# Kernel optimization log

Hardware: AMD Instinct MI355X
Metric: run time of the kernel (lower is better)

## Reference

```python
import jax, jax.numpy as jnp
import numpy as np

TEMP = 1.0
PRIOR = 0.2
THRESHOLD = 0.5
EPS = 1.1920929e-07  # torch float32 eps used by probs_to_logits / clamp_probs


def setup_inputs() -> dict:
    key = jax.random.key(0)
    k1, k2, k3, k4, k5 = jax.random.split(key, 5)
    B, L, D = 8, 8192, 256
    hidden = jax.random.normal(k1, (B, L, D), dtype=jnp.float32)
    # q/k projections are initialized to identity in the module; perturb slightly
    Wq = jnp.eye(D, dtype=jnp.float32) + 0.02 * jax.random.normal(k2, (D, D), dtype=jnp.float32)
    Wk = jnp.eye(D, dtype=jnp.float32) + 0.02 * jax.random.normal(k3, (D, D), dtype=jnp.float32)
    # uniform noise for the RelaxedBernoulli reparameterized sample
    noise = jax.random.uniform(k4, (B, L), dtype=jnp.float32)
    # ragged lengths -> contiguous attention mask (1s then 0s), as the module assumes
    lengths = jax.random.randint(k5, (B,), L // 2, L + 1)
    attention_mask = (jnp.arange(L)[None, :] < lengths[:, None]).astype(jnp.float32)
    return {"hidden": hidden, "Wq": Wq, "Wk": Wk, "noise": noise, "attention_mask": attention_mask}


def _binomial_loss(k, n, p):
    # -log Binomial(n, p).log_prob(k) / n
    logp = (jax.scipy.special.gammaln(n + 1.0)
            - jax.scipy.special.gammaln(k + 1.0)
            - jax.scipy.special.gammaln(n - k + 1.0)
            + k * jnp.log(p) + (n - k) * jnp.log1p(-p))
    return -logp / n


def reference(hidden, Wq, Wk, noise, attention_mask):
    B, L, D = hidden.shape
    # F.normalize along last dim (eps=1e-12), then linear projections (no bias)
    hn = hidden / jnp.maximum(jnp.linalg.norm(hidden, axis=-1, keepdims=True), 1e-12)
    q = jnp.einsum('bld,ed->ble', hn[:, :-1], Wq)
    k = jnp.einsum('bld,ed->ble', hn[:, 1:], Wk)
    cos_sim = jnp.sum(q * k, axis=-1)                      # [B, L-1]
    probs = jnp.clip((1.0 - cos_sim) * 0.5, 0.0, 1.0)
    probs = jnp.pad(probs, ((0, 0), (1, 0)), constant_values=1.0)  # boundary forced at t=0

    # RelaxedBernoulli(temp, probs).rsample() with externally supplied uniforms
    p = jnp.clip(probs, EPS, 1.0 - EPS)
    logits = jnp.log(p) - jnp.log1p(-p)
    u = jnp.clip(noise, EPS, 1.0 - EPS)
    soft = jax.nn.sigmoid((logits + jnp.log(u) - jnp.log1p(-u)) / TEMP)
    hard = (soft > THRESHOLD).astype(soft.dtype)
    hard = jax.lax.stop_gradient(hard - soft) + soft       # straight-through

    # mask out boundaries in padding; force a boundary at the last real token
    hard = hard * attention_mask
    pad_mask = attention_mask == 0
    first_pad = pad_mask & (jnp.cumsum(pad_mask.astype(jnp.int32), axis=1) == 1)
    last_real = jnp.roll(first_pad, shift=-1, axis=1).at[:, -1].set(False)
    hard = jnp.maximum(hard, last_real.astype(hard.dtype))

    # downsample: mean-pool tokens within each boundary-delimited segment.
    # boundary==1 starts a new segment; segment id = cumsum(hard) - 1.
    hard_bin = jax.lax.stop_gradient(hard) > 0.5
    seg = jnp.cumsum(hard_bin.astype(jnp.int32), axis=1) - 1
    seg = jnp.clip(seg, 0, L - 1)
    flat_seg = (seg + jnp.arange(B, dtype=jnp.int32)[:, None] * L).reshape(-1)  # [B*L]
    w = attention_mask.reshape(-1)                                              # pads excluded
    sums = jax.ops.segment_sum(hidden.reshape(-1, D) * w[:, None], flat_seg, num_segments=B * L)
    cnts = jax.ops.segment_sum(w, flat_seg, num_segments=B * L)
    pooled = (sums / (cnts + 1e-9)[:, None]).reshape(B, L, D)  # [B, S_max<=L, D], zero-padded

    n_b = jnp.sum(hard, axis=1)                  # boundaries per batch row
    num_boundaries = jnp.sum(n_b)
    total_positions = jnp.sum(attention_mask)
    # gathered mask values at kept positions are all 1 -> prefix-ones of length n_b
    shortened_attention_mask = (jnp.arange(L)[None, :]
                                < jax.lax.stop_gradient(n_b)[:, None]).astype(jnp.float32)
    loss = _binomial_loss(num_boundaries, total_positions, PRIOR)
    return pooled, loss, num_boundaries, total_positions, shortened_attention_mask
```

## Files before the change

### kernel.cpp

```cpp
#include <hip/hip_runtime.h>
#include <hip/hip_bf16.h>
#include <math.h>

#define L_SEQ 8192
#define B_BATCH 8
#define D_DIM 256
#define BL (B_BATCH * L_SEQ)
#define EPS_F 1.1920929e-07f

typedef __attribute__((ext_vector_type(8))) short short8;
typedef __attribute__((ext_vector_type(4))) float f32x4;
typedef __attribute__((ext_vector_type(4))) unsigned short u16x4;


__device__ inline unsigned short f2bf(float x) {
    __hip_bfloat16 b = __float2bfloat16(x);
    return *(unsigned short*)&b;
}
__device__ inline float bf2f(unsigned short u) {
    __hip_bfloat16 b = *(__hip_bfloat16*)&u;
    return __bfloat162float(b);
}

__global__ __launch_bounds__(256) void k_matMpack(
    const float* __restrict__ Wq, const float* __restrict__ Wk,
    unsigned short* __restrict__ Bpack) {
    __shared__ float Aq[64][33];
    __shared__ float Ak[64][17];
    const int f   = blockIdx.x;
    const int k8  = f >> 4, ct = f & 15;
    const int tid = threadIdx.x;
    const int n   = tid & 15;
    const int k   = tid >> 4;
    float a0 = 0.f, a1 = 0.f;
    for (int e0 = 0; e0 < 256; e0 += 64) {
        for (int i = tid; i < 64 * 32; i += 256) {
            const int e = i >> 5, d = i & 31;
            Aq[e][d] = Wq[(e0 + e) * 256 + k8 * 32 + d];
        }
        for (int i = tid; i < 64 * 16; i += 256) {
            const int e = i >> 4, d = i & 15;
            Ak[e][d] = Wk[(e0 + e) * 256 + ct * 16 + d];
        }
        __syncthreads();
#pragma unroll 8
        for (int e = 0; e < 64; ++e) {
            a0 += Aq[e][k] * Ak[e][n];
            a1 += Aq[e][k + 16] * Ak[e][n];
        }
        __syncthreads();
    }
    const int col = ct * 16 + n;
    const float M0 = a0 - ((k8 * 32 + k)      == col ? 1.0f : 0.0f);
    const float M1 = a1 - ((k8 * 32 + k + 16) == col ? 1.0f : 0.0f);
    const unsigned short h0 = f2bf(M0), h1 = f2bf(M1);
    const unsigned short l0 = f2bf(M0 - bf2f(h0)), l1 = f2bf(M1 - bf2f(h1));
    unsigned short* dstH = Bpack + (size_t)(k8 * 16 + ct) * 512;
    unsigned short* dstL = dstH + 128 * 512;
    const int q0 = k >> 3, j0 = k & 7;
    const int q1 = (k + 16) >> 3;
    dstH[(q0 * 16 + n) * 8 + j0] = h0;
    dstH[(q1 * 16 + n) * 8 + j0] = h1;
    dstL[(q0 * 16 + n) * 8 + j0] = l0;
    dstL[(q1 * 16 + n) * 8 + j0] = l1;
}

#define RS 264
#define MM(A,Bv,C) __builtin_amdgcn_mfma_f32_16x16x32_bf16((A),(Bv),(C),0,0,0)
#define MFMA16(V0,V1,V2,V3,BN) \
    acc[0][0]=MM(V0,BN##_0,acc[0][0]); acc[0][1]=MM(V0,BN##_1,acc[0][1]); \
    acc[0][2]=MM(V0,BN##_2,acc[0][2]); acc[0][3]=MM(V0,BN##_3,acc[0][3]); \
    acc[1][0]=MM(V1,BN##_0,acc[1][0]); acc[1][1]=MM(V1,BN##_1,acc[1][1]); \
    acc[1][2]=MM(V1,BN##_2,acc[1][2]); acc[1][3]=MM(V1,BN##_3,acc[1][3]); \
    acc[2][0]=MM(V2,BN##_0,acc[2][0]); acc[2][1]=MM(V2,BN##_1,acc[2][1]); \
    acc[2][2]=MM(V2,BN##_2,acc[2][2]); acc[2][3]=MM(V2,BN##_3,acc[2][3]); \
    acc[3][0]=MM(V3,BN##_0,acc[3][0]); acc[3][1]=MM(V3,BN##_1,acc[3][1]); \
    acc[3][2]=MM(V3,BN##_2,acc[3][2]); acc[3][3]=MM(V3,BN##_3,acc[3][3]);
#define LOADB(BN,S) \
    BN##_0 = Bld[(((S) * 16) + w4 + 0) * 64]; \
    BN##_1 = Bld[(((S) * 16) + w4 + 1) * 64]; \
    BN##_2 = Bld[(((S) * 16) + w4 + 2) * 64]; \
    BN##_3 = Bld[(((S) * 16) + w4 + 3) * 64];
#define STRIP_HL(S,BN) { \
    const int co = ((S) & 7) * 32; \
    const short8 hv0 = *(const short8*)(hA0 + co), hv1 = *(const short8*)(hA1 + co), \
                 hv2 = *(const short8*)(hA2 + co), hv3 = *(const short8*)(hA3 + co); \
    const short8 lv0 = *(const short8*)(lA0 + co), lv1 = *(const short8*)(lA1 + co), \
                 lv2 = *(const short8*)(lA2 + co), lv3 = *(const short8*)(lA3 + co); \
    MFMA16(hv0,hv1,hv2,hv3,BN); \
    MFMA16(lv0,lv1,lv2,lv3,BN); \
    LOADB(BN,(S)+3); }
#define STRIP_H(S,BN) { \
    const int co = ((S) & 7) * 32; \
    const short8 hv0 = *(const short8*)(hA0 + co), hv1 = *(const short8*)(hA1 + co), \
                 hv2 = *(const short8*)(hA2 + co), hv3 = *(const short8*)(hA3 + co); \
    MFMA16(hv0,hv1,hv2,hv3,BN); \
    if ((S) + 3 < 16) { LOADB(BN,(S)+3); } }

__global__ __launch_bounds__(256, 2) void k_cosmfma(
    const float* __restrict__ hidden, const unsigned short* __restrict__ Bpack,
    const float* __restrict__ noise, unsigned char* __restrict__ hard) {
    __shared__ __attribute__((aligned(16))) unsigned short hiA[65 * RS];
    __shared__ __attribute__((aligned(16))) unsigned short loA[65 * RS];
    __shared__ float Vpart[4][64];
    __shared__ float dots[64];

    const int tid  = threadIdx.x;
    const int lane = tid & 63;
    const int w    = tid >> 6;
    const int w16  = w * 16;
    const int w4   = w * 4;
    const int T0   = blockIdx.x * 64;

    const short8* __restrict__ Bld = (const short8*)Bpack + lane;

    short8 bA_0, bA_1, bA_2, bA_3, bB_0, bB_1, bB_2, bB_3, bC_0, bC_1, bC_2, bC_3;
    LOADB(bA, 0);
    LOADB(bB, 1);
    LOADB(bC, 2);

    {
        int tokA = T0 - 1 + w16; if (tokA < 0) tokA = 0;
        float4 vb0 = ((const float4*)hidden)[(size_t)tokA * 64 + lane];
        float4 vb1 = ((const float4*)hidden)[(size_t)(T0 + w16) * 64 + lane];
        float4 hp4 = {0.f, 0.f, 0.f, 0.f};
#pragma unroll 1
        for (int ii = 0; ii <= 16; ++ii) {
            const float4 vcur = vb0;
            vb0 = vb1;
            if (ii + 2 <= 16)
                vb1 = ((const float4*)hidden)[(size_t)(T0 + w16 + ii + 1) * 64 + lane];
            float ss = vcur.x * vcur.x + vcur.y * vcur.y + vcur.z * vcur.z + vcur.w * vcur.w;
#pragma unroll
            for (int sh = 32; sh >= 1; sh >>= 1) ss += __shfl_xor(ss, sh);
            const float inv = 1.0f / fmaxf(sqrtf(ss), 1e-12f);
            float4 h4;
            h4.x = vcur.x * inv; h4.y = vcur.y * inv;
            h4.z = vcur.z * inv; h4.w = vcur.w * inv;
            const unsigned short hx = f2bf(h4.x), hy = f2bf(h4.y),
                                 hz = f2bf(h4.z), hw2 = f2bf(h4.w);
            const u16x4 hv4 = {hx, hy, hz, hw2};
            const u16x4 lv4 = {f2bf(h4.x - bf2f(hx)), f2bf(h4.y - bf2f(hy)),
                               f2bf(h4.z - bf2f(hz)), f2bf(h4.w - bf2f(hw2))};
            const int i = w16 + ii;
            *(u16x4*)&hiA[i * RS + lane * 4] = hv4;
            *(u16x4*)&loA[i * RS + lane * 4] = lv4;
            if (ii > 0) {
                float pd = h4.x * hp4.x + h4.y * hp4.y + h4.z * hp4.z + h4.w * hp4.w;
#pragma unroll
                for (int sh = 32; sh >= 1; sh >>= 1) pd += __shfl_xor(pd, sh);
                if (lane == 0) dots[i - 1] = pd;
            }
            hp4 = h4;
        }
    }
    __syncthreads();

    const int m = lane & 15, q = lane >> 4;
    const unsigned short* __restrict__ hA0 = &hiA[(0  + m) * RS + q * 8];
    const unsigned short* __restrict__ hA1 = &hiA[(16 + m) * RS + q * 8];
    const unsigned short* __restrict__ hA2 = &hiA[(32 + m) * RS + q * 8];
    const unsigned short* __restrict__ hA3 = &hiA[(48 + m) * RS + q * 8];
    const unsigned short* __restrict__ lA0 = &loA[(0  + m) * RS + q * 8];
    const unsigned short* __restrict__ lA1 = &loA[(16 + m) * RS + q * 8];
    const unsigned short* __restrict__ lA2 = &loA[(32 + m) * RS + q * 8];
    const unsigned short* __restrict__ lA3 = &loA[(48 + m) * RS + q * 8];

    f32x4 acc[4][4];
#pragma unroll
    for (int af = 0; af < 4; ++af)
#pragma unroll
        for (int c = 0; c < 4; ++c) { f32x4 z = {0.f, 0.f, 0.f, 0.f}; acc[af][c] = z; }

    STRIP_HL(0, bA)  STRIP_HL(1, bB)  STRIP_HL(2, bC)  STRIP_HL(3, bA)
    STRIP_HL(4, bB)  STRIP_HL(5, bC)  STRIP_HL(6, bA)  STRIP_HL(7, bB)
    STRIP_H (8, bC)  STRIP_H (9, bA)  STRIP_H (10, bB) STRIP_H (11, bC)
    STRIP_H (12, bA) STRIP_H (13, bB) STRIP_H (14, bC) STRIP_H (15, bA)

#pragma unroll
    for (int af = 0; af < 4; ++af) {
#pragma unroll
        for (int r = 0; r < 4; ++r) {
            const int row = af * 16 + (q << 2) + r;
            const int ib  = (row + 1) * RS + w4 * 16 + m;
            float pp = acc[af][0][r] * (bf2f(hiA[ib     ]) + bf2f(loA[ib     ]))
                     + acc[af][1][r] * (bf2f(hiA[ib + 16]) + bf2f(loA[ib + 16]))
                     + acc[af][2][r] * (bf2f(hiA[ib + 32]) + bf2f(loA[ib + 32]))
                     + acc[af][3][r] * (bf2f(hiA[ib + 48]) + bf2f(loA[ib + 48]));
            pp += __shfl_xor(pp, 1);
            pp += __shfl_xor(pp, 2);
            pp += __shfl_xor(pp, 4);
            pp += __shfl_xor(pp, 8);
            if (m == 0) Vpart[w][row] = pp;
        }
    }
    __syncthreads();
    if (lane < 16) {
        const int rl = w16 + lane;
        const float part = Vpart[0][rl] + Vpart[1][rl] + Vpart[2][rl] + Vpart[3][rl];
        const int t = T0 + rl;
        const int l = t & (L_SEQ - 1);
        float p;
        if (l == 0) {
            p = 1.0f;
        } else {
            p = (1.0f - (part + dots[rl])) * 0.5f;
            p = fminf(fmaxf(p, 0.0f), 1.0f);
        }
        p = fminf(fmaxf(p, EPS_F), 1.0f - EPS_F);
        float u = noise[t];
        u = fminf(fmaxf(u, EPS_F), 1.0f - EPS_F);
        const float z = ((logf(p) - log1pf(-p)) + logf(u)) - log1pf(-u);
        hard[t] = (z > 0.0f) ? (unsigned char)1 : (unsigned char)0;
    }
}

__global__ __launch_bounds__(1024) void k_scan(
    const float* __restrict__ mask, const unsigned char* __restrict__ hard,
    int* __restrict__ starts, int* __restrict__ nb_arr,
    int* __restrict__ len_arr, float* __restrict__ out_short) {
    __shared__ int wsum[16];
    __shared__ int s_len;
    const int b = blockIdx.x, tid = threadIdx.x;
    const int lane = tid & 63, wv = tid >> 6;
    const int base = b * L_SEQ;

    const float4* m4 = (const float4*)(mask + base);
    const float4 va = m4[tid * 2], vb = m4[tid * 2 + 1];
    int cnt = (va.x != 0.f) + (va.y != 0.f) + (va.z != 0.f) + (va.w != 0.f)
            + (vb.x != 0.f) + (vb.y != 0.f) + (vb.z != 0.f) + (vb.w != 0.f);
#pragma unroll
    for (int sh = 32; sh >= 1; sh >>= 1) cnt += __shfl_xor(cnt, sh);
    if (lane == 0) wsum[wv] = cnt;
    __syncthreads();
    if (tid == 0) {
        int s = 0;
        for (int i = 0; i < 16; ++i) s += wsum[i];
        s_len = s;
    }
    __syncthreads();
    const int len = s_len;

    const int i0 = tid * 8;
    const uint2 hb = ((const uint2*)(hard + base))[tid];
    int c = 0;
    unsigned int bits = 0;
#pragma unroll
    for (int j = 0; j < 8; ++j) {
        const unsigned int byte = ((j < 4 ? hb.x : hb.y) >> (8 * (j & 3))) & 0xffu;
        int h = ((i0 + j) < len) ? (int)(byte != 0u) : 0;
        if (len < L_SEQ && (i0 + j) == len - 1) h = 1;
        bits |= (unsigned int)h << j;
        c += h;
    }
    int x = c;
#pragma unroll
    for (int ofs = 1; ofs < 64; ofs <<= 1) {
        const int t = __shfl_up(x, ofs);
        if (lane >= ofs) x += t;
    }
    if (lane == 63) wsum[wv] = x;
    __syncthreads();
    int woff = 0, nb = 0;
#pragma unroll
    for (int i = 0; i < 16; ++i) {
        const int t = wsum[i];
        nb += t;
        if (i < wv) woff += t;
    }
    int run = woff + x - c;
#pragma unroll
    for (int j = 0; j < 8; ++j)
        if ((bits >> j) & 1u) { starts[base + run] = i0 + j; ++run; }

    if (tid == 0) { nb_arr[b] = nb; len_arr[b] = len; }

    float4 o0, o1;
    o0.x = (i0 + 0) < nb ? 1.f : 0.f; o0.y = (i0 + 1) < nb ? 1.f : 0.f;
    o0.z = (i0 + 2) < nb ? 1.f : 0.f; o0.w = (i0 + 3) < nb ? 1.f : 0.f;
    o1.x = (i0 + 4) < nb ? 1.f : 0.f; o1.y = (i0 + 5) < nb ? 1.f : 0.f;
    o1.z = (i0 + 6) < nb ? 1.f : 0.f; o1.w = (i0 + 7) < nb ? 1.f : 0.f;
    float4* os4 = (float4*)(out_short + base);
    os4[tid * 2] = o0;
    os4[tid * 2 + 1] = o1;
}

__global__ __launch_bounds__(256) void k_pool(
    const float* __restrict__ hidden, const int* __restrict__ starts,
    const int* __restrict__ nb_arr, const int* __restrict__ len_arr,
    float* __restrict__ pooled) {
    const int tid  = threadIdx.x;
    const int lane = tid & 63;
    const int wid  = blockIdx.x * 4 + (tid >> 6);
    const int b    = wid >> 13;
    const int s    = wid & (L_SEQ - 1);
    const int nb   = nb_arr[b];

    float4 res = {0.f, 0.f, 0.f, 0.f};
    if (s < nb) {
        const int start = (s == 0) ? 0 : starts[b * L_SEQ + s];
        const int end   = (s + 1 < nb) ? starts[b * L_SEQ + s + 1] : len_arr[b];
        float4 acc = {0.f, 0.f, 0.f, 0.f};
        for (int t = start; t < end; ++t) {
            const float4 v = ((const float4*)hidden)[(b * L_SEQ + t) * 64 + lane];
            acc.x += v.x; acc.y += v.y; acc.z += v.z; acc.w += v.w;
        }
        const float cntf = (float)(end - start);
        res.x = acc.x / cntf; res.y = acc.y / cntf; res.z = acc.z / cntf; res.w = acc.w / cntf;
    }
    ((float4*)pooled)[(size_t)wid * 64 + lane] = res;
}

__global__ void k_final(const int* __restrict__ nb_arr, const int* __restrict__ len_arr,
                        float* __restrict__ out_scal) {
    if (threadIdx.x == 0) {
        int nb = 0, ln = 0;
        for (int b = 0; b < B_BATCH; ++b) { nb += nb_arr[b]; ln += len_arr[b]; }
        const double k = (double)nb, n = (double)ln;
        const double logp = lgamma(n + 1.0) - lgamma(k + 1.0) - lgamma(n - k + 1.0)
                            + k * log(0.2) + (n - k) * log(0.8);
        const double loss = -logp / n;
        out_scal[0] = (float)loss;
        out_scal[1] = (float)nb;
        out_scal[2] = (float)ln;
    }
}

extern "C" void kernel_launch(void* const* d_in, const int* in_sizes, int n_in,
                              void* d_out, int out_size, void* d_ws, size_t ws_size,
                              hipStream_t stream) {
    const float* hidden = (const float*)d_in[0];
    const float* Wq     = (const float*)d_in[1];
    const float* Wk     = (const float*)d_in[2];
    const float* noise  = (const float*)d_in[3];
    const float* mask   = (const float*)d_in[4];
    float* out = (float*)d_out;
    char* ws = (char*)d_ws;

    int*            starts = (int*)(ws);
    unsigned short* Bpack  = (unsigned short*)(ws + 262144);
    unsigned char*  hard   = (unsigned char*)(ws + 524288);
    int*            nb_arr = (int*)(ws + 589824);
    int*            len_arr= (int*)(ws + 589856);

    float* pooled = out;
    float* scal   = out + (size_t)BL * D_DIM;
    float* shortm = scal + 3;

    k_matMpack<<<128, 256, 0, stream>>>(Wq, Wk, Bpack);
    k_cosmfma <<<BL / 64, 256, 0, stream>>>(hidden, Bpack, noise, hard);
    k_scan    <<<B_BATCH, 1024, 0, stream>>>(mask, hard, starts, nb_arr, len_arr, shortm);
    k_pool    <<<BL / 4, 256, 0, stream>>>(hidden, starts, nb_arr, len_arr, pooled);
    k_final   <<<1, 64, 0, stream>>>(nb_arr, len_arr, scal);
}
```

Baseline: 189.3 us.

## Split cosine MFMA block across 8 waves with 2x4 wave tiling

Raises the k_cosmfma block size from 256 to 512 threads and splits the 64-row tile between two row groups of waves, so each wave computes 32 rows by 4 column groups instead of 64 rows. The normalize/pack prologue now gives 8 tokens per wave instead of 16. The goal is more waves per CU for latency hiding and fewer accumulators per wave (acc drops from 4x4 to 2x4) so occupancy can rise. In exchange, each B fragment is loaded twice per block, by two waves, and the larger block may limit residency through LDS use.

```diff
diff --git a/kernel.cpp b/kernel.cpp
--- a/kernel.cpp
+++ b/kernel.cpp
@@ -67,37 +67,30 @@
 
 #define RS 264
 #define MM(A,Bv,C) __builtin_amdgcn_mfma_f32_16x16x32_bf16((A),(Bv),(C),0,0,0)
-#define MFMA16(V0,V1,V2,V3,BN) \
+#define MFMA8(V0,V1,BN) \
     acc[0][0]=MM(V0,BN##_0,acc[0][0]); acc[0][1]=MM(V0,BN##_1,acc[0][1]); \
     acc[0][2]=MM(V0,BN##_2,acc[0][2]); acc[0][3]=MM(V0,BN##_3,acc[0][3]); \
     acc[1][0]=MM(V1,BN##_0,acc[1][0]); acc[1][1]=MM(V1,BN##_1,acc[1][1]); \
-    acc[1][2]=MM(V1,BN##_2,acc[1][2]); acc[1][3]=MM(V1,BN##_3,acc[1][3]); \
-    acc[2][0]=MM(V2,BN##_0,acc[2][0]); acc[2][1]=MM(V2,BN##_1,acc[2][1]); \
-    acc[2][2]=MM(V2,BN##_2,acc[2][2]); acc[2][3]=MM(V2,BN##_3,acc[2][3]); \
-    acc[3][0]=MM(V3,BN##_0,acc[3][0]); acc[3][1]=MM(V3,BN##_1,acc[3][1]); \
-    acc[3][2]=MM(V3,BN##_2,acc[3][2]); acc[3][3]=MM(V3,BN##_3,acc[3][3]);
+    acc[1][2]=MM(V1,BN##_2,acc[1][2]); acc[1][3]=MM(V1,BN##_3,acc[1][3]);
 #define LOADB(BN,S) \
-    BN##_0 = Bld[(((S) * 16) + w4 + 0) * 64]; \
-    BN##_1 = Bld[(((S) * 16) + w4 + 1) * 64]; \
-    BN##_2 = Bld[(((S) * 16) + w4 + 2) * 64]; \
-    BN##_3 = Bld[(((S) * 16) + w4 + 3) * 64];
+    BN##_0 = Bld[(((S) * 16) + wc4 + 0) * 64]; \
+    BN##_1 = Bld[(((S) * 16) + wc4 + 1) * 64]; \
+    BN##_2 = Bld[(((S) * 16) + wc4 + 2) * 64]; \
+    BN##_3 = Bld[(((S) * 16) + wc4 + 3) * 64];
 #define STRIP_HL(S,BN) { \
     const int co = ((S) & 7) * 32; \
-    const short8 hv0 = *(const short8*)(hA0 + co), hv1 = *(const short8*)(hA1 + co), \
-                 hv2 = *(const short8*)(hA2 + co), hv3 = *(const short8*)(hA3 + co); \
-    const short8 lv0 = *(const short8*)(lA0 + co), lv1 = *(const short8*)(lA1 + co), \
-                 lv2 = *(const short8*)(lA2 + co), lv3 = *(const short8*)(lA3 + co); \
-    MFMA16(hv0,hv1,hv2,hv3,BN); \
-    MFMA16(lv0,lv1,lv2,lv3,BN); \
-    LOADB(BN,(S)+3); }
+    const short8 hv0 = *(const short8*)(hA0 + co), hv1 = *(const short8*)(hA1 + co); \
+    const short8 lv0 = *(const short8*)(lA0 + co), lv1 = *(const short8*)(lA1 + co); \
+    MFMA8(hv0, hv1, BN); \
+    MFMA8(lv0, lv1, BN); \
+    LOADB(BN, (S) + 3); }
 #define STRIP_H(S,BN) { \
     const int co = ((S) & 7) * 32; \
-    const short8 hv0 = *(const short8*)(hA0 + co), hv1 = *(const short8*)(hA1 + co), \
-                 hv2 = *(const short8*)(hA2 + co), hv3 = *(const short8*)(hA3 + co); \
-    MFMA16(hv0,hv1,hv2,hv3,BN); \
-    if ((S) + 3 < 16) { LOADB(BN,(S)+3); } }
-
-__global__ __launch_bounds__(256, 2) void k_cosmfma(
+    const short8 hv0 = *(const short8*)(hA0 + co), hv1 = *(const short8*)(hA1 + co); \
+    MFMA8(hv0, hv1, BN); \
+    if ((S) + 3 < 16) { LOADB(BN, (S) + 3); } }
+
+__global__ __launch_bounds__(512, 4) void k_cosmfma(
     const float* __restrict__ hidden, const unsigned short* __restrict__ Bpack,
     const float* __restrict__ noise, unsigned char* __restrict__ hard) {
     __shared__ __attribute__((aligned(16))) unsigned short hiA[65 * RS];
@@ -108,8 +101,10 @@
     const int tid  = threadIdx.x;
     const int lane = tid & 63;
     const int w    = tid >> 6;
-    const int w16  = w * 16;
-    const int w4   = w * 4;
+    const int wr   = w >> 2;
+    const int wc   = w & 3;
+    const int wr32 = wr * 32;
+    const int wc4  = wc * 4;
     const int T0   = blockIdx.x * 64;
 
     const short8* __restrict__ Bld = (const short8*)Bpack + lane;
@@ -120,16 +115,17 @@
     LOADB(bC, 2);
 
     {
-        int tokA = T0 - 1 + w16; if (tokA < 0) tokA = 0;
+        const int r0 = w * 8;
+        int tokA = T0 - 1 + r0; if (tokA < 0) tokA = 0;
         float4 vb0 = ((const float4*)hidden)[(size_t)tokA * 64 + lane];
-        float4 vb1 = ((const float4*)hidden)[(size_t)(T0 + w16) * 64 + lane];
+        float4 vb1 = ((const float4*)hidden)[(size_t)(T0 + r0) * 64 + lane];
         float4 hp4 = {0.f, 0.f, 0.f, 0.f};
 #pragma unroll 1
-        for (int ii = 0; ii <= 16; ++ii) {
+        for (int ii = 0; ii <= 8; ++ii) {
             const float4 vcur = vb0;
             vb0 = vb1;
-            if (ii + 2 <= 16)
-                vb1 = ((const float4*)hidden)[(size_t)(T0 + w16 + ii + 1) * 64 + lane];
+            if (ii + 2 <= 8)
+                vb1 = ((const float4*)hidden)[(size_t)(T0 + r0 + ii + 1) * 64 + lane];
             float ss = vcur.x * vcur.x + vcur.y * vcur.y + vcur.z * vcur.z + vcur.w * vcur.w;
 #pragma unroll
             for (int sh = 32; sh >= 1; sh >>= 1) ss += __shfl_xor(ss, sh);
@@ -142,7 +138,7 @@
             const u16x4 hv4 = {hx, hy, hz, hw2};
             const u16x4 lv4 = {f2bf(h4.x - bf2f(hx)), f2bf(h4.y - bf2f(hy)),
                                f2bf(h4.z - bf2f(hz)), f2bf(h4.w - bf2f(hw2))};
-            const int i = w16 + ii;
+            const int i = r0 + ii;
             *(u16x4*)&hiA[i * RS + lane * 4] = hv4;
             *(u16x4*)&loA[i * RS + lane * 4] = lv4;
             if (ii > 0) {
@@ -157,18 +153,14 @@
     __syncthreads();
 
     const int m = lane & 15, q = lane >> 4;
-    const unsigned short* __restrict__ hA0 = &hiA[(0  + m) * RS + q * 8];
-    const unsigned short* __restrict__ hA1 = &hiA[(16 + m) * RS + q * 8];
-    const unsigned short* __restrict__ hA2 = &hiA[(32 + m) * RS + q * 8];
-    const unsigned short* __restrict__ hA3 = &hiA[(48 + m) * RS + q * 8];
-    const unsigned short* __restrict__ lA0 = &loA[(0  + m) * RS + q * 8];
-    const unsigned short* __restrict__ lA1 = &loA[(16 + m) * RS + q * 8];
-    const unsigned short* __restrict__ lA2 = &loA[(32 + m) * RS + q * 8];
-    const unsigned short* __restrict__ lA3 = &loA[(48 + m) * RS + q * 8];
-
-    f32x4 acc[4][4];
-#pragma unroll
-    for (int af = 0; af < 4; ++af)
+    const unsigned short* __restrict__ hA0 = &hiA[(wr32 +  0 + m) * RS + q * 8];
+    const unsigned short* __restrict__ hA1 = &hiA[(wr32 + 16 + m) * RS + q * 8];
+    const unsigned short* __restrict__ lA0 = &loA[(wr32 +  0 + m) * RS + q * 8];
+    const unsigned short* __restrict__ lA1 = &loA[(wr32 + 16 + m) * RS + q * 8];
+
+    f32x4 acc[2][4];
+#pragma unroll
+    for (int af = 0; af < 2; ++af)
 #pragma unroll
         for (int c = 0; c < 4; ++c) { f32x4 z = {0.f, 0.f, 0.f, 0.f}; acc[af][c] = z; }
 
@@ -178,11 +170,11 @@
     STRIP_H (12, bA) STRIP_H (13, bB) STRIP_H (14, bC) STRIP_H (15, bA)
 
 #pragma unroll
-    for (int af = 0; af < 4; ++af) {
+    for (int af = 0; af < 2; ++af) {
 #pragma unroll
         for (int r = 0; r < 4; ++r) {
-            const int row = af * 16 + (q << 2) + r;
-            const int ib  = (row + 1) * RS + w4 * 16 + m;
+            const int row = wr32 + af * 16 + (q << 2) + r;
+            const int ib  = (row + 1) * RS + wc4 * 16 + m;
             float pp = acc[af][0][r] * (bf2f(hiA[ib     ]) + bf2f(loA[ib     ]))
                      + acc[af][1][r] * (bf2f(hiA[ib + 16]) + bf2f(loA[ib + 16]))
                      + acc[af][2][r] * (bf2f(hiA[ib + 32]) + bf2f(loA[ib + 32]))
@@ -191,12 +183,12 @@
             pp += __shfl_xor(pp, 2);
             pp += __shfl_xor(pp, 4);
             pp += __shfl_xor(pp, 8);
-            if (m == 0) Vpart[w][row] = pp;
-        }
-    }
-    __syncthreads();
-    if (lane < 16) {
-        const int rl = w16 + lane;
+            if (m == 0) Vpart[wc][row] = pp;
+        }
+    }
+    __syncthreads();
+    if (tid < 64) {
+        const int rl = tid;
         const float part = Vpart[0][rl] + Vpart[1][rl] + Vpart[2][rl] + Vpart[3][rl];
         const int t = T0 + rl;
         const int l = t & (L_SEQ - 1);
@@ -348,7 +340,7 @@
     float* shortm = scal + 3;
 
     k_matMpack<<<128, 256, 0, stream>>>(Wq, Wk, Bpack);
-    k_cosmfma <<<BL / 64, 256, 0, stream>>>(hidden, Bpack, noise, hard);
+    k_cosmfma <<<BL / 64, 512, 0, stream>>>(hidden, Bpack, noise, hard);
     k_scan    <<<B_BATCH, 1024, 0, stream>>>(mask, hard, starts, nb_arr, len_arr, shortm);
     k_pool    <<<BL / 4, 256, 0, stream>>>(hidden, starts, nb_arr, len_arr, pooled);
     k_final   <<<1, 64, 0, stream>>>(nb_arr, len_arr, scal);
```

Result: faster. 180.6 us (-4.6%).
